# Performance work log

Measured on AMD Instinct MI355X. Metric: run time of the kernel, lower is better.

## Reference

```python
import jax, jax.numpy as jnp
import numpy as np

NUM_HEADS = 16

def setup_inputs() -> dict:
    key = jax.random.key(0)
    ks = jax.random.split(key, 6)
    B, S, D = 2, 2048, 1024
    scale = 1.0 / np.sqrt(D)
    x = jax.random.normal(ks[0], (B, S, D), dtype=jnp.float32)
    mask = jnp.tril(jnp.ones((S, S), dtype=jnp.int32))[None, None, :, :]  # causal [1,1,S,S]
    Wq = jax.random.normal(ks[1], (D, D), dtype=jnp.float32) * scale
    Wk = jax.random.normal(ks[2], (D, D), dtype=jnp.float32) * scale
    Wv = jax.random.normal(ks[3], (D, D), dtype=jnp.float32) * scale
    Wo = jax.random.normal(ks[4], (D, D), dtype=jnp.float32) * scale
    z = jnp.zeros((D,), dtype=jnp.float32)
    return {"x": x, "mask": mask, "Wq": Wq, "bq": z, "Wk": Wk, "bk": z,
            "Wv": Wv, "bv": z, "Wo": Wo, "bo": z}

def reference(x, mask, Wq, bq, Wk, bk, Wv, bv, Wo, bo):
    B, S, D = x.shape
    H = NUM_HEADS
    hd = D // H
    # torch Linear: y = x @ W.T + b
    def proj(W, b):
        return (x @ W.T + b).reshape(B, S, H, hd).transpose(0, 2, 1, 3)  # [B,H,S,hd]
    q = proj(Wq, bq)
    k = proj(Wk, bk)
    v = proj(Wv, bv)
    # NOTE: original module does NOT scale by 1/sqrt(d_k) -- faithful to source.
    scores = jnp.einsum('bhqd,bhkd->bhqk', q, k)  # [B,H,S,S]
    scores = jnp.where(mask == 0, jnp.float32(-10000.0), scores)
    attn = jax.nn.softmax(scores, axis=-1)
    # dropout omitted for deterministic reference (eval-mode equivalent)
    out = jnp.einsum('bhqk,bhkd->bhqd', attn, v)
    out = out.transpose(0, 2, 1, 3).reshape(B, S, D)
    return out @ Wo.T + bo
```

## Files before the change

kernel.cpp:

```cpp
#include <hip/hip_runtime.h>

#define S_LEN 2048
#define DM    1024
#define NHEAD 16
#define HDIM  64
#define NB    2
#define NROWS (NB * S_LEN)
#define RCP_LN2 1.44269504f

using f32x4  = __attribute__((ext_vector_type(4))) float;
using f16x8  = __attribute__((ext_vector_type(8))) _Float16;

__device__ __forceinline__ ushort f2h(float f) {
  return __builtin_bit_cast(ushort, (_Float16)f);
}
__device__ __forceinline__ float h2f(ushort u) {
  return (float)__builtin_bit_cast(_Float16, u);
}
__device__ __forceinline__ unsigned pkrtz(float a, float b) {
  return __builtin_bit_cast(unsigned, __builtin_amdgcn_cvt_pkrtz(a, b));
}
__device__ __forceinline__ float fexp2(float x) {
  return __builtin_amdgcn_exp2f(x);
}
__device__ __forceinline__ f32x4 mfma16(f16x8 a, f16x8 b, f32x4 c) {
  return __builtin_amdgcn_mfma_f32_16x16x32_f16(a, b, c, 0, 0, 0);
}
__device__ __forceinline__ void async16(const ushort* g, ushort* l) {
  __builtin_amdgcn_global_load_lds(
      (const __attribute__((address_space(1))) unsigned*)g,
      (__attribute__((address_space(3))) unsigned*)l, 16, 0, 0);
}

__device__ const int g_qi_tab[24] = {15,15,7,14,14,13,13,6,12,12,11,11,
                                     5,10,10,9,9,4,8,8,3,2,1,0};
__device__ const int g_hf_tab[24] = {0,1,2,0,1,0,1,2,0,1,0,1,
                                     2,0,1,0,1,2,0,1,2,2,2,2};

__global__ void tohalf5(const float* __restrict__ x,  const float* __restrict__ wq,
                        const float* __restrict__ wk, const float* __restrict__ wv,
                        const float* __restrict__ wo,
                        ushort* __restrict__ Xh, ushort* __restrict__ Wh,
                        ushort* __restrict__ Woh) {
  constexpr int X4 = (NROWS * DM) / 4;
  constexpr int W4 = (DM * DM) / 4;
  const size_t WN = (size_t)DM * DM;
  int i = blockIdx.x * 256 + threadIdx.x;
  const float4* src; ushort4* dst; int k;
  if (i < X4)               { src = (const float4*)x;  dst = (ushort4*)Xh;        k = i; }
  else if (i < X4 + W4)     { src = (const float4*)wq; dst = (ushort4*)Wh;        k = i - X4; }
  else if (i < X4 + 2*W4)   { src = (const float4*)wk; dst = (ushort4*)(Wh+WN);   k = i - X4 - W4; }
  else if (i < X4 + 3*W4)   { src = (const float4*)wv; dst = (ushort4*)(Wh+2*WN); k = i - X4 - 2*W4; }
  else                      { src = (const float4*)wo; dst = (ushort4*)Woh;       k = i - X4 - 3*W4; }
  float4 v = src[k];
  dst[k] = make_ushort4(f2h(v.x), f2h(v.y), f2h(v.z), f2h(v.w));
}

template<int EPI, int MFRAG, int NFRAG>
__global__ __launch_bounds__(256, 2)
void gemm_half(const ushort* __restrict__ A, const ushort* __restrict__ B,
               const float* __restrict__ biasQ, const float* __restrict__ biasK,
               const float* __restrict__ biasV,
               float* __restrict__ outF,
               ushort* __restrict__ Q, ushort* __restrict__ Kd,
               ushort* __restrict__ Vt, int Ncols)
{
  constexpr int KD = 1024;
  constexpr int BM = MFRAG * 32, BN = NFRAG * 32;
  constexpr int NCH = (BM + BN) / 8;
  constexpr int CPW = NCH / 4;
  __shared__ ushort sL[(BM + BN) * 64];
  const int t = threadIdx.x;
  const int w = t >> 6, l = t & 63;
  const int lr = l >> 4, lc = l & 15;
  const int wr = w >> 1, wc = w & 1;
  const int nwg = gridDim.x * gridDim.y;
  const int lin = blockIdx.y * gridDim.x + blockIdx.x;
  const int per8 = nwg >> 3;
  const int swz = (lin & 7) * per8 + (lin >> 3);
  const int i0 = (swz / gridDim.x) * BM, j0 = (swz % gridDim.x) * BN;

  const int srow = l >> 3;
  const int se   = ((l & 7) ^ srow) << 3;

  const ushort* sp[CPW];
#pragma unroll
  for (int ii = 0; ii < CPW; ++ii) {
    const int c = w * CPW + ii;
    sp[ii] = (c < BM / 8)
        ? A + (size_t)(i0 + c * 8 + srow) * KD + se
        : B + (size_t)(j0 + (c - BM / 8) * 8 + srow) * KD + se;
  }

  f32x4 acc[MFRAG][NFRAG] = {};

  for (int k0 = 0; k0 < KD; k0 += 64) {
#pragma unroll
    for (int ii = 0; ii < CPW; ++ii) {
      async16(sp[ii], &sL[(w * CPW + ii) * 512]);
      sp[ii] += 64;
    }
    asm volatile("s_waitcnt vmcnt(0)" ::: "memory");
    __syncthreads();
#pragma unroll
    for (int kk = 0; kk < 2; ++kk) {
      const int cb = (kk * 64 + lr * 16) ^ ((lc & 7) << 4);
      f16x8 a[MFRAG], b[NFRAG];
#pragma unroll
      for (int m = 0; m < MFRAG; ++m)
        a[m] = *(const f16x8*)&sL[(wr * MFRAG * 16 + m * 16 + lc) * 64 + (cb >> 1)];
#pragma unroll
      for (int n = 0; n < NFRAG; ++n)
        b[n] = *(const f16x8*)&sL[BM * 64 + (wc * NFRAG * 16 + n * 16 + lc) * 64 + (cb >> 1)];
      __builtin_amdgcn_s_setprio(1);
#pragma unroll
      for (int m = 0; m < MFRAG; ++m)
#pragma unroll
        for (int n = 0; n < NFRAG; ++n)
          acc[m][n] = mfma16(a[m], b[n], acc[m][n]);
      __builtin_amdgcn_s_setprio(0);
    }
    __syncthreads();
  }

#pragma unroll
  for (int m = 0; m < MFRAG; ++m)
#pragma unroll
    for (int n = 0; n < NFRAG; ++n) {
      const int jbase = j0 + wc * NFRAG * 16 + n * 16;
      const int ibase = i0 + wr * MFRAG * 16 + m * 16 + lr * 4;
      if constexpr (EPI == 0) {
        const int region = jbase >> 10;
        const int jc0 = jbase & 1023;
        const int h = jc0 >> 6, d0 = jc0 & 63;
        const int b = ibase >> 11, s0 = ibase & 2047;
        const size_t bh = (size_t)(b * NHEAD + h);
        if (region == 0) {
          float bb = biasQ[jc0 + lc];
#pragma unroll
          for (int r = 0; r < 4; ++r)
            Q[(bh * S_LEN + s0 + r) * HDIM + d0 + lc] =
                f2h((acc[m][n][r] + bb) * RCP_LN2);
        } else if (region == 1) {
          float bb = biasK[jc0 + lc];
#pragma unroll
          for (int r = 0; r < 4; ++r)
            Kd[(bh * S_LEN + s0 + r) * HDIM + d0 + lc] = f2h(acc[m][n][r] + bb);
        } else {
          float bb = biasV[jc0 + lc];
          ushort4 pv = make_ushort4(f2h(acc[m][n][0] + bb), f2h(acc[m][n][1] + bb),
                                    f2h(acc[m][n][2] + bb), f2h(acc[m][n][3] + bb));
          *(ushort4*)&Vt[(bh * HDIM + d0 + lc) * S_LEN + s0] = pv;
        }
      } else {
#pragma unroll
        for (int r = 0; r < 4; ++r)
          outF[(size_t)(ibase + r) * Ncols + jbase + lc] =
              acc[m][n][r] + biasQ[jbase + lc];
      }
    }
}

__global__ __launch_bounds__(256, 3)
void attn_kernel(const ushort* __restrict__ Qp, const ushort* __restrict__ Kp,
                 const ushort* __restrict__ Vt, ushort* __restrict__ O,
                 ushort* __restrict__ Pacc, float* __restrict__ Pml)
{
  __shared__ ushort sKV[2][2 * 64 * 64];
  __shared__ ushort Plds[4][2][16][72];
  const int blk = blockIdx.x;
  const int c = blk & 255, s3 = blk >> 8;
  const int rank = (s3 == 0) ? c : ((s3 == 1) ? 511 - c : 512 + c);
  const int ty = rank >> 5, bh = rank & 31;
  const int qi = g_qi_tab[ty], hf = g_hf_tab[ty];
  const int nkt = 2 * qi + 2;
  const int kt0 = (hf == 1) ? (nkt >> 1) : 0;
  const int kt1 = (hf == 0) ? (nkt >> 1) : nkt;

  const int t = threadIdx.x, w = t >> 6, l = t & 63;
  const int g = l >> 4, q = l & 15;
  const size_t base = (size_t)bh * S_LEN * HDIM;
  const int q0w = qi * 128 + w * 32;

  const int srow = l >> 3;
  const int se   = ((l & 7) ^ srow) << 3;

  const int sel = w >> 1;
  const ushort* sp[4];
  const int sadv = (sel == 0) ? 64 * HDIM : 64;
#pragma unroll
  for (int ii = 0; ii < 4; ++ii) {
    const int sub = (w * 4 + ii) & 7;
    sp[ii] = (sel == 0)
        ? Kp + base + (size_t)(kt0 * 64 + sub * 8 + srow) * HDIM + se
        : Vt + ((size_t)bh * HDIM + sub * 8 + srow) * S_LEN + kt0 * 64 + se;
  }

  auto stage = [&](int buf) {
#pragma unroll
    for (int ii = 0; ii < 4; ++ii) {
      const int sub = (w * 4 + ii) & 7;
      async16(sp[ii], &sKV[buf][sel * 4096 + sub * 512]);
      sp[ii] += sadv;
    }
  };

  f16x8 bQ[2][2];
#pragma unroll
  for (int u = 0; u < 2; ++u)
#pragma unroll
    for (int ks = 0; ks < 2; ++ks)
      bQ[u][ks] = *(const f16x8*)(Qp + base +
                  (size_t)(q0w + u * 16 + q) * HDIM + ks * 32 + g * 8);

  f32x4 oacc[2][4] = {};
  float m[2] = {-3e38f, -3e38f}, lsum[2] = {0.f, 0.f};

  stage(0);
  asm volatile("s_waitcnt vmcnt(0)" ::: "memory");
  __syncthreads();
  int cur = 0;

  for (int kt = kt0; kt < kt1; ++kt) {
    if (kt + 1 < kt1) stage(cur ^ 1);

    if (kt * 64 <= q0w + 31) {
      f32x4 s[2][4] = {};
      __builtin_amdgcn_s_setprio(1);
#pragma unroll
      for (int ks = 0; ks < 2; ++ks) {
        const int cb = (((ks * 64 + g * 16) ^ ((q & 7) << 4)) >> 1);
#pragma unroll
        for (int n = 0; n < 4; ++n) {
          f16x8 kf = *(const f16x8*)&sKV[cur][(n * 16 + q) * 64 + cb];
          s[0][n] = mfma16(kf, bQ[0][ks], s[0][n]);
          s[1][n] = mfma16(kf, bQ[1][ks], s[1][n]);
        }
      }
      __builtin_amdgcn_s_setprio(0);
#pragma unroll
      for (int u = 0; u < 2; ++u) {
        if (kt * 64 + 63 > q0w + u * 16) {
          const int qg = q0w + u * 16 + q;
#pragma unroll
          for (int n = 0; n < 4; ++n)
#pragma unroll
            for (int r = 0; r < 4; ++r) {
              int kg = kt * 64 + n * 16 + g * 4 + r;
              if (kg > qg) s[u][n][r] = -1e30f;
            }
        }
      }
      float pm[2];
#pragma unroll
      for (int u = 0; u < 2; ++u) {
        float p = -3e38f;
#pragma unroll
        for (int n = 0; n < 4; ++n)
          p = fmaxf(p, fmaxf(fmaxf(s[u][n][0], s[u][n][1]),
                             fmaxf(s[u][n][2], s[u][n][3])));
        pm[u] = p;
      }
#pragma unroll
      for (int u = 0; u < 2; ++u) {
        if (__any(pm[u] > m[u] + 8.0f)) {
          float pf = pm[u];
          pf = fmaxf(pf, __shfl_xor(pf, 16));
          pf = fmaxf(pf, __shfl_xor(pf, 32));
          float mnew = fmaxf(m[u], pf);
          float sc = fexp2(m[u] - mnew);
          m[u] = mnew;
          float scr[4];
#pragma unroll
          for (int r = 0; r < 4; ++r) scr[r] = __shfl(sc, g * 4 + r);
#pragma unroll
          for (int dt = 0; dt < 4; ++dt)
#pragma unroll
            for (int r = 0; r < 4; ++r) oacc[u][dt][r] *= scr[r];
          lsum[u] *= sc;
        }
      }
#pragma unroll
      for (int u = 0; u < 2; ++u) {
        float rs = 0.f;
#pragma unroll
        for (int n = 0; n < 4; ++n)
#pragma unroll
          for (int r = 0; r < 4; ++r) {
            float pe = fexp2(s[u][n][r] - m[u]);
            s[u][n][r] = pe;
            rs += pe;
          }
        lsum[u] += rs;
      }
#pragma unroll
      for (int u = 0; u < 2; ++u)
#pragma unroll
        for (int n = 0; n < 4; ++n) {
          uint2 pk = make_uint2(pkrtz(s[u][n][0], s[u][n][1]),
                                pkrtz(s[u][n][2], s[u][n][3]));
          *(uint2*)&Plds[w][u][q][n * 16 + g * 4] = pk;
        }
      __builtin_amdgcn_s_setprio(1);
#pragma unroll
      for (int ks = 0; ks < 2; ++ks) {
        const int cb = (((ks * 64 + g * 16) ^ ((q & 7) << 4)) >> 1);
        f16x8 ap0 = *(const f16x8*)&Plds[w][0][q][ks * 32 + g * 8];
        f16x8 ap1 = *(const f16x8*)&Plds[w][1][q][ks * 32 + g * 8];
#pragma unroll
        for (int dt = 0; dt < 4; ++dt) {
          f16x8 bv = *(const f16x8*)&sKV[cur][4096 + (dt * 16 + q) * 64 + cb];
          oacc[0][dt] = mfma16(ap0, bv, oacc[0][dt]);
          oacc[1][dt] = mfma16(ap1, bv, oacc[1][dt]);
        }
      }
      __builtin_amdgcn_s_setprio(0);
    }
    asm volatile("s_waitcnt vmcnt(0)" ::: "memory");
    __syncthreads();
    cur ^= 1;
  }

#pragma unroll
  for (int u = 0; u < 2; ++u) {
    lsum[u] += __shfl_xor(lsum[u], 16);
    lsum[u] += __shfl_xor(lsum[u], 32);
  }

  if (hf == 2) {
    const int b = bh >> 4, h = bh & 15;
#pragma unroll
    for (int u = 0; u < 2; ++u) {
      float lsr[4];
#pragma unroll
      for (int r = 0; r < 4; ++r)
        lsr[r] = __builtin_amdgcn_rcpf(__shfl(lsum[u], g * 4 + r));
#pragma unroll
      for (int dt = 0; dt < 4; ++dt)
#pragma unroll
        for (int r = 0; r < 4; ++r) {
          int qg = q0w + u * 16 + g * 4 + r;
          O[((size_t)b * S_LEN + qg) * DM + h * HDIM + dt * 16 + q] =
              f2h(oacc[u][dt][r] * lsr[r]);
        }
    }
  } else {
    const int pidx = (bh * 8 + (qi - 8)) * 2 + hf;
    ushort* po = Pacc + (size_t)pidx * (128 * 64);
#pragma unroll
    for (int u = 0; u < 2; ++u) {
#pragma unroll
      for (int dt = 0; dt < 4; ++dt)
#pragma unroll
        for (int r = 0; r < 4; ++r)
          po[(w * 32 + u * 16 + g * 4 + r) * 64 + dt * 16 + q] = f2h(oacc[u][dt][r]);
      if (g == 0) {
        Pml[(size_t)pidx * 256 + (w * 32 + u * 16 + q) * 2]     = m[u];
        Pml[(size_t)pidx * 256 + (w * 32 + u * 16 + q) * 2 + 1] = lsum[u];
      }
    }
  }
}

__global__ void combine_kernel(const ushort* __restrict__ Pacc,
                               const float* __restrict__ Pml,
                               ushort* __restrict__ O)
{
  int gid = blockIdx.x * 256 + threadIdx.x;
  int cq  = gid & 15;
  int rr  = (gid >> 4) & 1023;
  int bh  = gid >> 14;
  int qi = 8 + (rr >> 7), qr = rr & 127;
  int p0 = (bh * 8 + (qi - 8)) * 2;
  float m1 = Pml[(size_t)p0 * 256 + qr * 2];
  float l1 = Pml[(size_t)p0 * 256 + qr * 2 + 1];
  float m2 = Pml[(size_t)(p0 + 1) * 256 + qr * 2];
  float l2 = Pml[(size_t)(p0 + 1) * 256 + qr * 2 + 1];
  ushort4 o1 = *(const ushort4*)&Pacc[(size_t)p0 * 8192 + qr * 64 + cq * 4];
  ushort4 o2 = *(const ushort4*)&Pacc[(size_t)(p0 + 1) * 8192 + qr * 64 + cq * 4];
  float mf = fmaxf(m1, m2);
  float e1 = fexp2(m1 - mf), e2 = fexp2(m2 - mf);
  float rl = __builtin_amdgcn_rcpf(l1 * e1 + l2 * e2);
  ushort4 o;
  o.x = f2h((h2f(o1.x) * e1 + h2f(o2.x) * e2) * rl);
  o.y = f2h((h2f(o1.y) * e1 + h2f(o2.y) * e2) * rl);
  o.z = f2h((h2f(o1.z) * e1 + h2f(o2.z) * e2) * rl);
  o.w = f2h((h2f(o1.w) * e1 + h2f(o2.w) * e2) * rl);
  int b = bh >> 4, h = bh & 15;
  *(ushort4*)&O[((size_t)b * S_LEN + qi * 128 + qr) * DM + h * HDIM + cq * 4] = o;
}

extern "C" void kernel_launch(void* const* d_in, const int* in_sizes, int n_in,
                              void* d_out, int out_size, void* d_ws, size_t ws_size,
                              hipStream_t stream)
{
  const float* x  = (const float*)d_in[0];
  const float* Wq = (const float*)d_in[2];
  const float* bq = (const float*)d_in[3];
  const float* Wk = (const float*)d_in[4];
  const float* bk = (const float*)d_in[5];
  const float* Wv = (const float*)d_in[6];
  const float* bv = (const float*)d_in[7];
  const float* Wo = (const float*)d_in[8];
  const float* bo = (const float*)d_in[9];
  float* out = (float*)d_out;

  char* ws = (char*)d_ws;
  size_t off = 0;
  auto alloc = [&](size_t bytes) { char* p = ws + off; off += bytes; return p; };
  const size_t XN = (size_t)NROWS * DM;
  const size_t WN = (size_t)DM * DM;

  ushort* Xh  = (ushort*)alloc(XN * 2);
  ushort* Wh  = (ushort*)alloc(3 * WN * 2);
  ushort* Woh = (ushort*)alloc(WN * 2);
  ushort* Qb  = (ushort*)alloc(XN * 2);
  ushort* Kb  = (ushort*)alloc(XN * 2);
  ushort* Vt  = (ushort*)alloc(XN * 2);
  ushort* Ob  = (ushort*)alloc(XN * 2);
  ushort* Pacc = (ushort*)alloc((size_t)512 * 128 * 64 * 2);
  float*  Pml  = (float*)alloc((size_t)512 * 256 * 4);
  (void)ws_size; (void)in_sizes; (void)n_in; (void)out_size;

  const int total4 = (int)(XN / 4 + 4 * (WN / 4));
  tohalf5<<<total4 / 256, 256, 0, stream>>>(x, Wq, Wk, Wv, Wo, Xh, Wh, Woh);

  gemm_half<0, 4, 4><<<dim3(24, 32), 256, 0, stream>>>(
      Xh, Wh, bq, bk, bv, nullptr, Qb, Kb, Vt, 3072);
  attn_kernel<<<768, 256, 0, stream>>>(Qb, Kb, Vt, Ob, Pacc, Pml);
  combine_kernel<<<2048, 256, 0, stream>>>(Pacc, Pml, Ob);
  gemm_half<1, 2, 4><<<dim3(8, 64), 256, 0, stream>>>(
      Ob, Woh, bo, nullptr, nullptr, out, nullptr, nullptr, nullptr, 1024);
}
```

Baseline: 99.25 us.

## Add dedicated 256x256-tile double-buffered QKV GEMM with 512-thread blocks

Replaces the templated QKV projection GEMM with a dedicated kernel. It uses 256x256 output tiles, 8 waves per block, and double-buffered async global-to-LDS staging with explicit vmcnt waits and barriers. The larger tiles cut global and LDS reload traffic per FLOP, and the prefetch overlaps loads with MFMA work. The trade-off is a grid of only 192 blocks and about 128KB of LDS per block, which may leave CUs idle and limit occupancy. The output-projection GEMM template is simplified to drop the now-unused QKV epilogue.

```diff
diff --git a/kernel.cpp b/kernel.cpp
--- a/kernel.cpp
+++ b/kernel.cpp
@@ -56,14 +56,122 @@
   dst[k] = make_ushort4(f2h(v.x), f2h(v.y), f2h(v.z), f2h(v.w));
 }
 
-template<int EPI, int MFRAG, int NFRAG>
+__global__ __launch_bounds__(512, 2)
+void gemm_qkv(const ushort* __restrict__ A, const ushort* __restrict__ B,
+              const float* __restrict__ biasQ, const float* __restrict__ biasK,
+              const float* __restrict__ biasV,
+              ushort* __restrict__ Q, ushort* __restrict__ Kd,
+              ushort* __restrict__ Vt)
+{
+  constexpr int KD = 1024;
+  __shared__ ushort sL[2][32768];
+  const int t = threadIdx.x;
+  const int w = t >> 6, l = t & 63;
+  const int lr = l >> 4, lc = l & 15;
+  const int wr = w >> 2, wc = w & 3;
+  const int lin = blockIdx.y * gridDim.x + blockIdx.x;
+  const int swz = (lin & 7) * 24 + (lin >> 3);
+  const int i0 = (swz / 12) * 256, j0 = (swz % 12) * 256;
+
+  const int srow = t >> 3;
+  const int scol = ((t & 7) ^ (srow & 7)) << 3;
+  const ushort* pa = A + (size_t)(i0 + srow) * KD + scol;
+  const ushort* pb = B + (size_t)(j0 + srow) * KD + scol;
+
+  auto STAGE = [&](int s, int kt) {
+    const int k0 = kt * 64;
+#pragma unroll
+    for (int j = 0; j < 4; ++j) {
+      async16(pa + (size_t)j * 64 * KD + k0, &sL[s][(t + j * 512) * 8]);
+      async16(pb + (size_t)j * 64 * KD + k0, &sL[s][16384 + (t + j * 512) * 8]);
+    }
+  };
+
+  f32x4 acc[8][4] = {};
+
+  STAGE(0, 0);
+  for (int kt = 0; kt < 16; ++kt) {
+    const int s = kt & 1;
+    if (kt + 1 < 16) {
+      STAGE(s ^ 1, kt + 1);
+      asm volatile("s_waitcnt vmcnt(8)" ::: "memory");
+    } else {
+      asm volatile("s_waitcnt vmcnt(0)" ::: "memory");
+    }
+    __builtin_amdgcn_s_barrier();
+
+    f16x8 b[4][2];
+#pragma unroll
+    for (int ph = 0; ph < 4; ++ph) {
+      f16x8 a[2][2];
+#pragma unroll
+      for (int m2 = 0; m2 < 2; ++m2)
+#pragma unroll
+        for (int kk = 0; kk < 2; ++kk) {
+          const int row = wr * 128 + (ph * 2 + m2) * 16 + lc;
+          const int cb = (kk * 64 + lr * 16) ^ ((lc & 7) << 4);
+          a[m2][kk] = *(const f16x8*)&sL[s][row * 64 + (cb >> 1)];
+        }
+      if (ph == 0) {
+#pragma unroll
+        for (int nf = 0; nf < 4; ++nf)
+#pragma unroll
+          for (int kk = 0; kk < 2; ++kk) {
+            const int row = wc * 64 + nf * 16 + lc;
+            const int cb = (kk * 64 + lr * 16) ^ ((lc & 7) << 4);
+            b[nf][kk] = *(const f16x8*)&sL[s][16384 + row * 64 + (cb >> 1)];
+          }
+      }
+      __builtin_amdgcn_s_barrier();
+      __builtin_amdgcn_s_setprio(1);
+#pragma unroll
+      for (int m2 = 0; m2 < 2; ++m2)
+#pragma unroll
+        for (int nf = 0; nf < 4; ++nf)
+#pragma unroll
+          for (int kk = 0; kk < 2; ++kk)
+            acc[ph * 2 + m2][nf] = mfma16(a[m2][kk], b[nf][kk], acc[ph * 2 + m2][nf]);
+      __builtin_amdgcn_s_setprio(0);
+      __builtin_amdgcn_s_barrier();
+    }
+  }
+
+#pragma unroll
+  for (int mf = 0; mf < 8; ++mf)
+#pragma unroll
+    for (int nf = 0; nf < 4; ++nf) {
+      const int jbase = j0 + wc * 64 + nf * 16;
+      const int ibase = i0 + wr * 128 + mf * 16 + lr * 4;
+      const int region = jbase >> 10;
+      const int jc0 = jbase & 1023;
+      const int h = jc0 >> 6, d0 = jc0 & 63;
+      const int bb_ = ibase >> 11, s0 = ibase & 2047;
+      const size_t bh = (size_t)(bb_ * NHEAD + h);
+      if (region == 0) {
+        float bb = biasQ[jc0 + lc];
+#pragma unroll
+        for (int r = 0; r < 4; ++r)
+          Q[(bh * S_LEN + s0 + r) * HDIM + d0 + lc] =
+              f2h((acc[mf][nf][r] + bb) * RCP_LN2);
+      } else if (region == 1) {
+        float bb = biasK[jc0 + lc];
+#pragma unroll
+        for (int r = 0; r < 4; ++r)
+          Kd[(bh * S_LEN + s0 + r) * HDIM + d0 + lc] = f2h(acc[mf][nf][r] + bb);
+      } else {
+        float bb = biasV[jc0 + lc];
+        ushort4 pv = make_ushort4(f2h(acc[mf][nf][0] + bb), f2h(acc[mf][nf][1] + bb),
+                                  f2h(acc[mf][nf][2] + bb), f2h(acc[mf][nf][3] + bb));
+        *(ushort4*)&Vt[(bh * HDIM + d0 + lc) * S_LEN + s0] = pv;
+      }
+    }
+}
+
+template<int MFRAG, int NFRAG>
 __global__ __launch_bounds__(256, 2)
 void gemm_half(const ushort* __restrict__ A, const ushort* __restrict__ B,
-               const float* __restrict__ biasQ, const float* __restrict__ biasK,
-               const float* __restrict__ biasV,
-               float* __restrict__ outF,
-               ushort* __restrict__ Q, ushort* __restrict__ Kd,
-               ushort* __restrict__ Vt, int Ncols)
+               const float* __restrict__ bias, float* __restrict__ outF,
+               int Ncols)
 {
   constexpr int KD = 1024;
   constexpr int BM = MFRAG * 32, BN = NFRAG * 32;
@@ -129,35 +237,10 @@
     for (int n = 0; n < NFRAG; ++n) {
       const int jbase = j0 + wc * NFRAG * 16 + n * 16;
       const int ibase = i0 + wr * MFRAG * 16 + m * 16 + lr * 4;
-      if constexpr (EPI == 0) {
-        const int region = jbase >> 10;
-        const int jc0 = jbase & 1023;
-        const int h = jc0 >> 6, d0 = jc0 & 63;
-        const int b = ibase >> 11, s0 = ibase & 2047;
-        const size_t bh = (size_t)(b * NHEAD + h);
-        if (region == 0) {
-          float bb = biasQ[jc0 + lc];
-#pragma unroll
-          for (int r = 0; r < 4; ++r)
-            Q[(bh * S_LEN + s0 + r) * HDIM + d0 + lc] =
-                f2h((acc[m][n][r] + bb) * RCP_LN2);
-        } else if (region == 1) {
-          float bb = biasK[jc0 + lc];
-#pragma unroll
-          for (int r = 0; r < 4; ++r)
-            Kd[(bh * S_LEN + s0 + r) * HDIM + d0 + lc] = f2h(acc[m][n][r] + bb);
-        } else {
-          float bb = biasV[jc0 + lc];
-          ushort4 pv = make_ushort4(f2h(acc[m][n][0] + bb), f2h(acc[m][n][1] + bb),
-                                    f2h(acc[m][n][2] + bb), f2h(acc[m][n][3] + bb));
-          *(ushort4*)&Vt[(bh * HDIM + d0 + lc) * S_LEN + s0] = pv;
-        }
-      } else {
-#pragma unroll
-        for (int r = 0; r < 4; ++r)
-          outF[(size_t)(ibase + r) * Ncols + jbase + lc] =
-              acc[m][n][r] + biasQ[jbase + lc];
-      }
+#pragma unroll
+      for (int r = 0; r < 4; ++r)
+        outF[(size_t)(ibase + r) * Ncols + jbase + lc] =
+            acc[m][n][r] + bias[jbase + lc];
     }
 }
 
@@ -425,10 +508,8 @@
   const int total4 = (int)(XN / 4 + 4 * (WN / 4));
   tohalf5<<<total4 / 256, 256, 0, stream>>>(x, Wq, Wk, Wv, Wo, Xh, Wh, Woh);
 
-  gemm_half<0, 4, 4><<<dim3(24, 32), 256, 0, stream>>>(
-      Xh, Wh, bq, bk, bv, nullptr, Qb, Kb, Vt, 3072);
+  gemm_qkv<<<dim3(12, 16), 512, 0, stream>>>(Xh, Wh, bq, bk, bv, Qb, Kb, Vt);
   attn_kernel<<<768, 256, 0, stream>>>(Qb, Kb, Vt, Ob, Pacc, Pml);
   combine_kernel<<<2048, 256, 0, stream>>>(Pacc, Pml, Ob);
-  gemm_half<1, 2, 4><<<dim3(8, 64), 256, 0, stream>>>(
-      Ob, Woh, bo, nullptr, nullptr, out, nullptr, nullptr, nullptr, 1024);
-}
+  gemm_half<2, 4><<<dim3(8, 64), 256, 0, stream>>>(Ob, Woh, bo, out, 1024);
+}
```

After: 109.4 us. 10.2% more time.
